# Optimization experiments

Measured on AMD Instinct MI355X. Metric: run time of the kernel, lower is better.

## Reference

```python
import jax, jax.numpy as jnp
import numpy as np

M = 4096        # node_num
NN = 16         # neighbors per node (nn_num)
G = 4           # graph_num
IN_F = 32
OUT_F = 32
LOC_F = 8
LHID = 128
B = 16


def setup_inputs() -> dict:
    key = jax.random.key(0)
    ks = jax.random.split(key, 9)
    return {
        "x": jax.random.normal(ks[0], (B, M, IN_F), jnp.float32),
        "maps": jax.random.normal(ks[1], (M * NN, LOC_F), jnp.float32),
        "L_idx": jax.random.randint(ks[2], (M * NN,), 0, M * M, jnp.int64 if jax.config.jax_enable_x64 else jnp.int32),
        "W1": jax.random.normal(ks[3], (G, LHID, LOC_F), jnp.float32) * 0.1,
        "b1": jax.random.normal(ks[4], (G, LHID), jnp.float32) * 0.1,
        "W2": jax.random.normal(ks[5], (G, LHID), jnp.float32) * 0.1,
        "b2": jax.random.normal(ks[6], (G,), jnp.float32) * 0.1,
        "Wx": jax.random.normal(ks[7], (G, IN_F, OUT_F), jnp.float32) * 0.1,
        "bx": jax.random.normal(ks[8], (OUT_F,), jnp.float32) * 0.1,
    }


def reference(x, maps, L_idx, W1, b1, W2, b2, Wx, bx):
    # x: (B, m, in_f); maps: (m*nn, loc); L_idx: (m*nn,) indices into flat m*m
    g, lhid, loc = W1.shape
    bsz, m, f = x.shape
    nn_num = maps.shape[0] // m

    # per-graph tiny MLP over all node-neighbor pairs, vectorized over graphs
    h = jnp.tanh(jnp.einsum("nl,ghl->gnh", maps, W1) + b1[:, None, :])   # (g, m*nn, lhid)
    ctx = jnp.einsum("gnh,gh->gn", h, W2) + b2[:, None]                   # (g, m*nn)
    # softmax over the nn_num neighbors of each node (F.softmax on (m, nn) -> dim=1)
    attn = jax.nn.softmax(ctx.reshape(g, m, nn_num), axis=-1).reshape(g, m * nn_num)

    # scatter attention into dense per-graph Laplacians: L[L_idx] = attn
    L = jnp.zeros((g, m * m), attn.dtype).at[:, L_idx].set(attn).reshape(g, m, m)

    # XeLayer: out = sum_g (L_g @ x) @ Wx_g + bx
    agg = jnp.einsum("gij,bjf->gbif", L, x)          # (g, B, m, f)
    out = jnp.einsum("gbif,gfo->bio", agg, Wx) + bx   # (B, m, out_f)
    return out
```

## Files before the change

### kernel.cpp

```cpp
#include <hip/hip_runtime.h>

#define M_NODES 4096
#define NN_NUM 16
#define G_NUM 4
#define IN_F 32
#define OUT_F 32
#define LOC_F 8
#define LHID 128
#define B_SZ 16
#define NPAIR 65536
#define ROWCAP 64

typedef __attribute__((ext_vector_type(8))) short short8;
typedef __attribute__((ext_vector_type(4))) float f32x4;

static __device__ __forceinline__ unsigned short f2bf(float f) {
  union { float f; unsigned u; } c; c.f = f;
  const unsigned r = c.u + 0x7FFFu + ((c.u >> 16) & 1u);
  return (unsigned short)(r >> 16);
}
static __device__ __forceinline__ float bfhi2f(unsigned u) {
  union { unsigned u; float f; } c; c.u = u & 0xFFFF0000u; return c.f;
}
static __device__ __forceinline__ float bflo2f(unsigned u) {
  union { unsigned u; float f; } c; c.u = u << 16; return c.f;
}

__global__ void __launch_bounds__(256)
prep_kernel(const float* __restrict__ maps,
            const float* __restrict__ W1,
            const float* __restrict__ b1,
            const float* __restrict__ W2,
            const float* __restrict__ Wx,
            uint4* __restrict__ mapsbf4,
            ushort* __restrict__ w1bf,
            float2* __restrict__ b1w2,
            ushort4* __restrict__ wxf4,
            unsigned* __restrict__ rowcount) {
  const int idx = blockIdx.x * 256 + threadIdx.x;

  {
    const float4 a = *reinterpret_cast<const float4*>(maps + (size_t)idx * 8);
    const float4 b = *reinterpret_cast<const float4*>(maps + (size_t)idx * 8 + 4);
    uint4 r;
    r.x = (unsigned)f2bf(a.x) | ((unsigned)f2bf(a.y) << 16);
    r.y = (unsigned)f2bf(a.z) | ((unsigned)f2bf(a.w) << 16);
    r.z = (unsigned)f2bf(b.x) | ((unsigned)f2bf(b.y) << 16);
    r.w = (unsigned)f2bf(b.z) | ((unsigned)f2bf(b.w) << 16);
    mapsbf4[idx] = r;
  }

  if (idx < G_NUM * LHID * LOC_F) w1bf[idx] = f2bf(W1[idx]);
  if (idx < G_NUM * LHID)
    b1w2[idx] = make_float2(b1[idx], -2.0f * W2[idx]);

  if (idx < 512) {
    const int l = idx & 63, tile = (idx >> 6) & 1, g = idx >> 7;
    const int lo = l & 15, hi = l >> 4;
    ushort4 r0, r1;
    r0.x = f2bf(Wx[g * 1024 + (hi * 8 + 0) * 32 + tile * 16 + lo]);
    r0.y = f2bf(Wx[g * 1024 + (hi * 8 + 1) * 32 + tile * 16 + lo]);
    r0.z = f2bf(Wx[g * 1024 + (hi * 8 + 2) * 32 + tile * 16 + lo]);
    r0.w = f2bf(Wx[g * 1024 + (hi * 8 + 3) * 32 + tile * 16 + lo]);
    r1.x = f2bf(Wx[g * 1024 + (hi * 8 + 4) * 32 + tile * 16 + lo]);
    r1.y = f2bf(Wx[g * 1024 + (hi * 8 + 5) * 32 + tile * 16 + lo]);
    r1.z = f2bf(Wx[g * 1024 + (hi * 8 + 6) * 32 + tile * 16 + lo]);
    r1.w = f2bf(Wx[g * 1024 + (hi * 8 + 7) * 32 + tile * 16 + lo]);
    wxf4[idx * 2] = r0;
    wxf4[idx * 2 + 1] = r1;
  }

  if (idx < M_NODES) rowcount[idx] = 0;
}

__global__ void __launch_bounds__(256)
mlp_kernel(const float4* __restrict__ x4,
           ushort4* __restrict__ xb4,
           const ushort* __restrict__ mapsbf,
           const ushort* __restrict__ w1bf,
           const float2* __restrict__ b1w2,
           const int* __restrict__ L_idx,
           unsigned* __restrict__ rowcount,
           uint2* __restrict__ csr_jn,
           float4* __restrict__ csr_a) {
  const int t = threadIdx.x;
  const int l = t & 63;
  const int g = t >> 6;
  const int node = blockIdx.x;
  const int lo = l & 15;
  const int hi = l >> 4;

  __shared__ float sAttn[G_NUM][16];

  {
    const int idx = blockIdx.x * 256 + t;
    if (idx < 524288) {
      const float4 v = x4[idx];
      ushort4 o;
      o.x = f2bf(v.x); o.y = f2bf(v.y); o.z = f2bf(v.z); o.w = f2bf(v.w);
      xb4[idx] = o;
    }
  }

  short8 aF = {0, 0, 0, 0, 0, 0, 0, 0};
  if (hi == 0)
    aF = *reinterpret_cast<const short8*>(mapsbf + ((size_t)node * 16 + lo) * 8);

  short8 bF[8];
  float2 bw[8];
#pragma unroll
  for (int tile = 0; tile < 8; ++tile) {
    bF[tile] = *reinterpret_cast<const short8*>(
        w1bf + ((size_t)(g * LHID + tile * 16 + lo)) * 8);
    bw[tile] = b1w2[g * LHID + tile * 16 + lo];
  }

  float cr[4] = {0.f, 0.f, 0.f, 0.f};
#pragma unroll
  for (int tile = 0; tile < 8; ++tile) {
    f32x4 c = {bw[tile].x, bw[tile].x, bw[tile].x, bw[tile].x};
    c = __builtin_amdgcn_mfma_f32_16x16x32_bf16(aF, bF[tile], c, 0, 0, 0);
    const float nw2 = bw[tile].y;
#pragma unroll
    for (int r = 0; r < 4; ++r) {
      const float e = __expf(c[r] + c[r]);
      cr[r] = fmaf(nw2, __builtin_amdgcn_rcpf(e + 1.0f), cr[r]);
    }
  }

#pragma unroll
  for (int m = 1; m <= 8; m <<= 1) {
    cr[0] += __shfl_xor(cr[0], m, 64);
    cr[1] += __shfl_xor(cr[1], m, 64);
    cr[2] += __shfl_xor(cr[2], m, 64);
    cr[3] += __shfl_xor(cr[3], m, 64);
  }

  float mx = fmaxf(fmaxf(cr[0], cr[1]), fmaxf(cr[2], cr[3]));
  mx = fmaxf(mx, __shfl_xor(mx, 16, 64));
  mx = fmaxf(mx, __shfl_xor(mx, 32, 64));
  const float e0 = __expf(cr[0] - mx), e1 = __expf(cr[1] - mx);
  const float e2 = __expf(cr[2] - mx), e3 = __expf(cr[3] - mx);
  float s = e0 + e1 + e2 + e3;
  s += __shfl_xor(s, 16, 64);
  s += __shfl_xor(s, 32, 64);
  const float inv = __builtin_amdgcn_rcpf(s);

  if (lo == 0) {
    sAttn[g][hi * 4 + 0] = e0 * inv;
    sAttn[g][hi * 4 + 1] = e1 * inv;
    sAttn[g][hi * 4 + 2] = e2 * inv;
    sAttn[g][hi * 4 + 3] = e3 * inv;
  }
  __syncthreads();

  if (t < 16) {
    const int n = node * 16 + t;
    const unsigned pos = (unsigned)L_idx[n];
    const unsigned i = pos >> 12;
    const unsigned j = pos & (M_NODES - 1);
    const unsigned slot = atomicAdd(&rowcount[i], 1u);
    if (slot < ROWCAP) {
      csr_jn[(size_t)i * ROWCAP + slot] = make_uint2(j, (unsigned)n);
      csr_a[(size_t)i * ROWCAP + slot] =
          make_float4(sAttn[0][t], sAttn[1][t], sAttn[2][t], sAttn[3][t]);
    }
  }
}

__global__ void __launch_bounds__(256)
gather_kernel(const ushort* __restrict__ xbf,
              const uint2* __restrict__ csr_jn,
              const float4* __restrict__ csr_a,
              const unsigned* __restrict__ rowcount,
              const ushort* __restrict__ wxf,
              const float* __restrict__ bx,
              float* __restrict__ out) {
  const int t = threadIdx.x;
  const int l = t & 63;
  const int i = blockIdx.x * 4 + (t >> 6);
  const int lo = l & 15;
  const int hi = l >> 4;

  short8 bF[G_NUM][2];
#pragma unroll
  for (int g = 0; g < G_NUM; ++g)
#pragma unroll
    for (int tile = 0; tile < 2; ++tile)
      bF[g][tile] = *reinterpret_cast<const short8*>(
          wxf + ((size_t)((g * 2 + tile) * 64 + l)) * 8);

  const unsigned cnt = min(rowcount[i], (unsigned)ROWCAP);
  const uint2 e = csr_jn[(size_t)i * ROWCAP + l];
  float4 aq = csr_a[(size_t)i * ROWCAP + l];
  const bool valid = (unsigned)l < cnt;
  unsigned myj = valid ? e.x : 0xFFFFFFFFu;
  const unsigned myn = valid ? e.y : 0u;

  bool alive = valid;
  for (unsigned d = 0; d < cnt; ++d) {
    const unsigned jd = __shfl(myj, (int)d);
    const unsigned nd = __shfl(myn, (int)d);
    if (jd == myj && nd > myn) alive = false;
  }
  if (!alive) { aq.x = 0.f; aq.y = 0.f; aq.z = 0.f; aq.w = 0.f; }
  myj &= (M_NODES - 1u);

  float acc[G_NUM][8];
#pragma unroll
  for (int g = 0; g < G_NUM; ++g)
#pragma unroll
    for (int q = 0; q < 8; ++q) acc[g][q] = 0.f;

  const uint4* xrow = reinterpret_cast<const uint4*>(xbf) + hi;
  const size_t browbase = (size_t)lo * M_NODES * 4;

  for (unsigned s = 0; s < cnt; ++s) {
    const unsigned js = __shfl(myj, (int)s);
    const float w0 = __shfl(aq.x, (int)s);
    const float w1 = __shfl(aq.y, (int)s);
    const float w2 = __shfl(aq.z, (int)s);
    const float w3 = __shfl(aq.w, (int)s);
    const uint4 xv = xrow[browbase + (size_t)js * 4];
    float xf[8];
    xf[0] = bflo2f(xv.x); xf[1] = bfhi2f(xv.x);
    xf[2] = bflo2f(xv.y); xf[3] = bfhi2f(xv.y);
    xf[4] = bflo2f(xv.z); xf[5] = bfhi2f(xv.z);
    xf[6] = bflo2f(xv.w); xf[7] = bfhi2f(xv.w);
#pragma unroll
    for (int q = 0; q < 8; ++q) {
      acc[0][q] = fmaf(w0, xf[q], acc[0][q]);
      acc[1][q] = fmaf(w1, xf[q], acc[1][q]);
      acc[2][q] = fmaf(w2, xf[q], acc[2][q]);
      acc[3][q] = fmaf(w3, xf[q], acc[3][q]);
    }
  }

  f32x4 c0 = {0.f, 0.f, 0.f, 0.f};
  f32x4 c1 = {0.f, 0.f, 0.f, 0.f};
#pragma unroll
  for (int g = 0; g < G_NUM; ++g) {
    short8 aF;
#pragma unroll
    for (int q = 0; q < 8; ++q) aF[q] = (short)f2bf(acc[g][q]);
    c0 = __builtin_amdgcn_mfma_f32_16x16x32_bf16(aF, bF[g][0], c0, 0, 0, 0);
    c1 = __builtin_amdgcn_mfma_f32_16x16x32_bf16(aF, bF[g][1], c1, 0, 0, 0);
  }

  const float bias0 = bx[lo];
  const float bias1 = bx[16 + lo];
#pragma unroll
  for (int r = 0; r < 4; ++r) {
    const int b = hi * 4 + r;
    float* op = out + ((size_t)b * M_NODES + i) * OUT_F;
    op[lo] = c0[r] + bias0;
    op[16 + lo] = c1[r] + bias1;
  }
}

extern "C" void kernel_launch(void* const* d_in, const int* in_sizes, int n_in,
                              void* d_out, int out_size, void* d_ws, size_t ws_size,
                              hipStream_t stream) {
  const float* x    = (const float*)d_in[0];
  const float* maps = (const float*)d_in[1];
  const int*   L_idx = (const int*)d_in[2];
  const float* W1   = (const float*)d_in[3];
  const float* b1   = (const float*)d_in[4];
  const float* W2   = (const float*)d_in[5];
  const float* Wx   = (const float*)d_in[7];
  const float* bx   = (const float*)d_in[8];
  float* out = (float*)d_out;

  char* ws = (char*)d_ws;
  float4*   csr_a    = (float4*)ws;
  uint2*    csr_jn   = (uint2*)(ws + (4u << 20));
  ushort*   xbf      = (ushort*)(ws + (6u << 20));
  unsigned* rowcount = (unsigned*)(ws + (10u << 20));
  ushort*   mapsbf   = (ushort*)(ws + (11u << 20));
  ushort*   w1bf     = (ushort*)(ws + (12u << 20));
  float2*   b1w2     = (float2*)(ws + (12u << 20) + (32u << 10));
  ushort*   wxf      = (ushort*)(ws + (12u << 20) + (64u << 10));

  prep_kernel<<<256, 256, 0, stream>>>(
      maps, W1, b1, W2, Wx,
      (uint4*)mapsbf, w1bf, b1w2, (ushort4*)wxf, rowcount);
  mlp_kernel<<<M_NODES, 256, 0, stream>>>(
      (const float4*)x, (ushort4*)xbf, mapsbf, w1bf, b1w2, L_idx,
      rowcount, csr_jn, csr_a);
  gather_kernel<<<M_NODES / 4, 256, 0, stream>>>(
      xbf, csr_jn, csr_a, rowcount, wxf, bx, out);
}
```

Measured before the change: 44.18 us.

## Process two nodes per MLP block and batch gather loads in groups of eight

```diff
diff --git a/kernel.cpp b/kernel.cpp
--- a/kernel.cpp
+++ b/kernel.cpp
@@ -86,25 +86,26 @@
   const int t = threadIdx.x;
   const int l = t & 63;
   const int g = t >> 6;
-  const int node = blockIdx.x;
+  const int node0 = blockIdx.x * 2;
   const int lo = l & 15;
   const int hi = l >> 4;
 
-  __shared__ float sAttn[G_NUM][16];
+  __shared__ float sAttn[G_NUM][2][16];
 
   {
     const int idx = blockIdx.x * 256 + t;
-    if (idx < 524288) {
-      const float4 v = x4[idx];
-      ushort4 o;
-      o.x = f2bf(v.x); o.y = f2bf(v.y); o.z = f2bf(v.z); o.w = f2bf(v.w);
-      xb4[idx] = o;
-    }
-  }
-
-  short8 aF = {0, 0, 0, 0, 0, 0, 0, 0};
-  if (hi == 0)
-    aF = *reinterpret_cast<const short8*>(mapsbf + ((size_t)node * 16 + lo) * 8);
+    const float4 v = x4[idx];
+    ushort4 o;
+    o.x = f2bf(v.x); o.y = f2bf(v.y); o.z = f2bf(v.z); o.w = f2bf(v.w);
+    xb4[idx] = o;
+  }
+
+  short8 aF0 = {0, 0, 0, 0, 0, 0, 0, 0};
+  short8 aF1 = {0, 0, 0, 0, 0, 0, 0, 0};
+  if (hi == 0) {
+    aF0 = *reinterpret_cast<const short8*>(mapsbf + ((size_t)node0 * 16 + lo) * 8);
+    aF1 = *reinterpret_cast<const short8*>(mapsbf + ((size_t)(node0 + 1) * 16 + lo) * 8);
+  }
 
   short8 bF[8];
   float2 bw[8];
@@ -115,47 +116,67 @@
     bw[tile] = b1w2[g * LHID + tile * 16 + lo];
   }
 
-  float cr[4] = {0.f, 0.f, 0.f, 0.f};
+  float cr0[4] = {0.f, 0.f, 0.f, 0.f};
+  float cr1[4] = {0.f, 0.f, 0.f, 0.f};
 #pragma unroll
   for (int tile = 0; tile < 8; ++tile) {
-    f32x4 c = {bw[tile].x, bw[tile].x, bw[tile].x, bw[tile].x};
-    c = __builtin_amdgcn_mfma_f32_16x16x32_bf16(aF, bF[tile], c, 0, 0, 0);
+    const float b1v = bw[tile].x;
     const float nw2 = bw[tile].y;
+    f32x4 c0 = {b1v, b1v, b1v, b1v};
+    f32x4 c1 = {b1v, b1v, b1v, b1v};
+    c0 = __builtin_amdgcn_mfma_f32_16x16x32_bf16(aF0, bF[tile], c0, 0, 0, 0);
+    c1 = __builtin_amdgcn_mfma_f32_16x16x32_bf16(aF1, bF[tile], c1, 0, 0, 0);
 #pragma unroll
     for (int r = 0; r < 4; ++r) {
-      const float e = __expf(c[r] + c[r]);
-      cr[r] = fmaf(nw2, __builtin_amdgcn_rcpf(e + 1.0f), cr[r]);
+      const float e0 = exp2f(c0[r] * 2.885390082f);
+      const float e1 = exp2f(c1[r] * 2.885390082f);
+      cr0[r] = fmaf(nw2, __builtin_amdgcn_rcpf(e0 + 1.0f), cr0[r]);
+      cr1[r] = fmaf(nw2, __builtin_amdgcn_rcpf(e1 + 1.0f), cr1[r]);
     }
   }
 
 #pragma unroll
   for (int m = 1; m <= 8; m <<= 1) {
-    cr[0] += __shfl_xor(cr[0], m, 64);
-    cr[1] += __shfl_xor(cr[1], m, 64);
-    cr[2] += __shfl_xor(cr[2], m, 64);
-    cr[3] += __shfl_xor(cr[3], m, 64);
-  }
-
-  float mx = fmaxf(fmaxf(cr[0], cr[1]), fmaxf(cr[2], cr[3]));
-  mx = fmaxf(mx, __shfl_xor(mx, 16, 64));
-  mx = fmaxf(mx, __shfl_xor(mx, 32, 64));
-  const float e0 = __expf(cr[0] - mx), e1 = __expf(cr[1] - mx);
-  const float e2 = __expf(cr[2] - mx), e3 = __expf(cr[3] - mx);
-  float s = e0 + e1 + e2 + e3;
-  s += __shfl_xor(s, 16, 64);
-  s += __shfl_xor(s, 32, 64);
-  const float inv = __builtin_amdgcn_rcpf(s);
+#pragma unroll
+    for (int r = 0; r < 4; ++r) {
+      cr0[r] += __shfl_xor(cr0[r], m, 64);
+      cr1[r] += __shfl_xor(cr1[r], m, 64);
+    }
+  }
+
+  float mx0 = fmaxf(fmaxf(cr0[0], cr0[1]), fmaxf(cr0[2], cr0[3]));
+  float mx1 = fmaxf(fmaxf(cr1[0], cr1[1]), fmaxf(cr1[2], cr1[3]));
+  mx0 = fmaxf(mx0, __shfl_xor(mx0, 16, 64));
+  mx1 = fmaxf(mx1, __shfl_xor(mx1, 16, 64));
+  mx0 = fmaxf(mx0, __shfl_xor(mx0, 32, 64));
+  mx1 = fmaxf(mx1, __shfl_xor(mx1, 32, 64));
+  float e00 = __expf(cr0[0] - mx0), e01 = __expf(cr0[1] - mx0);
+  float e02 = __expf(cr0[2] - mx0), e03 = __expf(cr0[3] - mx0);
+  float e10 = __expf(cr1[0] - mx1), e11 = __expf(cr1[1] - mx1);
+  float e12 = __expf(cr1[2] - mx1), e13 = __expf(cr1[3] - mx1);
+  float s0 = e00 + e01 + e02 + e03;
+  float s1 = e10 + e11 + e12 + e13;
+  s0 += __shfl_xor(s0, 16, 64); s1 += __shfl_xor(s1, 16, 64);
+  s0 += __shfl_xor(s0, 32, 64); s1 += __shfl_xor(s1, 32, 64);
+  const float inv0 = __builtin_amdgcn_rcpf(s0);
+  const float inv1 = __builtin_amdgcn_rcpf(s1);
 
   if (lo == 0) {
-    sAttn[g][hi * 4 + 0] = e0 * inv;
-    sAttn[g][hi * 4 + 1] = e1 * inv;
-    sAttn[g][hi * 4 + 2] = e2 * inv;
-    sAttn[g][hi * 4 + 3] = e3 * inv;
+    sAttn[g][0][hi * 4 + 0] = e00 * inv0;
+    sAttn[g][0][hi * 4 + 1] = e01 * inv0;
+    sAttn[g][0][hi * 4 + 2] = e02 * inv0;
+    sAttn[g][0][hi * 4 + 3] = e03 * inv0;
+    sAttn[g][1][hi * 4 + 0] = e10 * inv1;
+    sAttn[g][1][hi * 4 + 1] = e11 * inv1;
+    sAttn[g][1][hi * 4 + 2] = e12 * inv1;
+    sAttn[g][1][hi * 4 + 3] = e13 * inv1;
   }
   __syncthreads();
 
-  if (t < 16) {
-    const int n = node * 16 + t;
+  if (t < 32) {
+    const int ns = t >> 4;
+    const int p = t & 15;
+    const int n = (node0 + ns) * 16 + p;
     const unsigned pos = (unsigned)L_idx[n];
     const unsigned i = pos >> 12;
     const unsigned j = pos & (M_NODES - 1);
@@ -163,7 +184,8 @@
     if (slot < ROWCAP) {
       csr_jn[(size_t)i * ROWCAP + slot] = make_uint2(j, (unsigned)n);
       csr_a[(size_t)i * ROWCAP + slot] =
-          make_float4(sAttn[0][t], sAttn[1][t], sAttn[2][t], sAttn[3][t]);
+          make_float4(sAttn[0][ns][p], sAttn[1][ns][p],
+                      sAttn[2][ns][p], sAttn[3][ns][p]);
     }
   }
 }
@@ -182,14 +204,6 @@
   const int lo = l & 15;
   const int hi = l >> 4;
 
-  short8 bF[G_NUM][2];
-#pragma unroll
-  for (int g = 0; g < G_NUM; ++g)
-#pragma unroll
-    for (int tile = 0; tile < 2; ++tile)
-      bF[g][tile] = *reinterpret_cast<const short8*>(
-          wxf + ((size_t)((g * 2 + tile) * 64 + l)) * 8);
-
   const unsigned cnt = min(rowcount[i], (unsigned)ROWCAP);
   const uint2 e = csr_jn[(size_t)i * ROWCAP + l];
   float4 aq = csr_a[(size_t)i * ROWCAP + l];
@@ -215,26 +229,42 @@
   const uint4* xrow = reinterpret_cast<const uint4*>(xbf) + hi;
   const size_t browbase = (size_t)lo * M_NODES * 4;
 
-  for (unsigned s = 0; s < cnt; ++s) {
-    const unsigned js = __shfl(myj, (int)s);
-    const float w0 = __shfl(aq.x, (int)s);
-    const float w1 = __shfl(aq.y, (int)s);
-    const float w2 = __shfl(aq.z, (int)s);
-    const float w3 = __shfl(aq.w, (int)s);
-    const uint4 xv = xrow[browbase + (size_t)js * 4];
-    float xf[8];
-    xf[0] = bflo2f(xv.x); xf[1] = bfhi2f(xv.x);
-    xf[2] = bflo2f(xv.y); xf[3] = bfhi2f(xv.y);
-    xf[4] = bflo2f(xv.z); xf[5] = bfhi2f(xv.z);
-    xf[6] = bflo2f(xv.w); xf[7] = bfhi2f(xv.w);
-#pragma unroll
-    for (int q = 0; q < 8; ++q) {
-      acc[0][q] = fmaf(w0, xf[q], acc[0][q]);
-      acc[1][q] = fmaf(w1, xf[q], acc[1][q]);
-      acc[2][q] = fmaf(w2, xf[q], acc[2][q]);
-      acc[3][q] = fmaf(w3, xf[q], acc[3][q]);
+  const unsigned cnt8 = (cnt + 7u) & ~7u;
+  for (unsigned base = 0; base < cnt8; base += 8) {
+    unsigned js[8];
+    uint4 v[8];
+#pragma unroll
+    for (int k = 0; k < 8; ++k) js[k] = __shfl(myj, (int)(base + k));
+#pragma unroll
+    for (int k = 0; k < 8; ++k) v[k] = xrow[browbase + (size_t)js[k] * 4];
+#pragma unroll
+    for (int k = 0; k < 8; ++k) {
+      const float w0 = __shfl(aq.x, (int)(base + k));
+      const float w1 = __shfl(aq.y, (int)(base + k));
+      const float w2 = __shfl(aq.z, (int)(base + k));
+      const float w3 = __shfl(aq.w, (int)(base + k));
+      float xf[8];
+      xf[0] = bflo2f(v[k].x); xf[1] = bfhi2f(v[k].x);
+      xf[2] = bflo2f(v[k].y); xf[3] = bfhi2f(v[k].y);
+      xf[4] = bflo2f(v[k].z); xf[5] = bfhi2f(v[k].z);
+      xf[6] = bflo2f(v[k].w); xf[7] = bfhi2f(v[k].w);
+#pragma unroll
+      for (int q = 0; q < 8; ++q) {
+        acc[0][q] = fmaf(w0, xf[q], acc[0][q]);
+        acc[1][q] = fmaf(w1, xf[q], acc[1][q]);
+        acc[2][q] = fmaf(w2, xf[q], acc[2][q]);
+        acc[3][q] = fmaf(w3, xf[q], acc[3][q]);
+      }
     }
   }
+
+  short8 bF[G_NUM][2];
+#pragma unroll
+  for (int g = 0; g < G_NUM; ++g)
+#pragma unroll
+    for (int tile = 0; tile < 2; ++tile)
+      bF[g][tile] = *reinterpret_cast<const short8*>(
+          wxf + ((size_t)((g * 2 + tile) * 64 + l)) * 8);
 
   f32x4 c0 = {0.f, 0.f, 0.f, 0.f};
   f32x4 c1 = {0.f, 0.f, 0.f, 0.f};
@@ -284,7 +314,7 @@
   prep_kernel<<<256, 256, 0, stream>>>(
       maps, W1, b1, W2, Wx,
       (uint4*)mapsbf, w1bf, b1w2, (ushort4*)wxf, rowcount);
-  mlp_kernel<<<M_NODES, 256, 0, stream>>>(
+  mlp_kernel<<<M_NODES / 2, 256, 0, stream>>>(
       (const float4*)x, (ushort4*)xbf, mapsbf, w1bf, b1w2, L_idx,
       rowcount, csr_jn, csr_a);
   gather_kernel<<<M_NODES / 4, 256, 0, stream>>>(
```

Result: slower. 50.21 us (+13.6%).

## Pipeline gather row loads through LDS with async global_load_lds staging

Applied to the files above, without the earlier changes.

```diff
diff --git a/kernel.cpp b/kernel.cpp
--- a/kernel.cpp
+++ b/kernel.cpp
@@ -10,9 +10,12 @@
 #define B_SZ 16
 #define NPAIR 65536
 #define ROWCAP 64
+#define STAGE_D 4
 
 typedef __attribute__((ext_vector_type(8))) short short8;
 typedef __attribute__((ext_vector_type(4))) float f32x4;
+typedef const unsigned __attribute__((address_space(1))) gbl_u32;
+typedef unsigned __attribute__((address_space(3))) lds_u32;
 
 static __device__ __forceinline__ unsigned short f2bf(float f) {
   union { float f; unsigned u; } c; c.f = f;
@@ -118,12 +121,13 @@
   float cr[4] = {0.f, 0.f, 0.f, 0.f};
 #pragma unroll
   for (int tile = 0; tile < 8; ++tile) {
-    f32x4 c = {bw[tile].x, bw[tile].x, bw[tile].x, bw[tile].x};
+    const float b1v = bw[tile].x;
+    const float nw2 = bw[tile].y;
+    f32x4 c = {b1v, b1v, b1v, b1v};
     c = __builtin_amdgcn_mfma_f32_16x16x32_bf16(aF, bF[tile], c, 0, 0, 0);
-    const float nw2 = bw[tile].y;
 #pragma unroll
     for (int r = 0; r < 4; ++r) {
-      const float e = __expf(c[r] + c[r]);
+      const float e = exp2f(c[r] * 2.885390082f);
       cr[r] = fmaf(nw2, __builtin_amdgcn_rcpf(e + 1.0f), cr[r]);
     }
   }
@@ -178,17 +182,12 @@
               float* __restrict__ out) {
   const int t = threadIdx.x;
   const int l = t & 63;
-  const int i = blockIdx.x * 4 + (t >> 6);
+  const int w = t >> 6;
+  const int i = blockIdx.x * 4 + w;
   const int lo = l & 15;
   const int hi = l >> 4;
 
-  short8 bF[G_NUM][2];
-#pragma unroll
-  for (int g = 0; g < G_NUM; ++g)
-#pragma unroll
-    for (int tile = 0; tile < 2; ++tile)
-      bF[g][tile] = *reinterpret_cast<const short8*>(
-          wxf + ((size_t)((g * 2 + tile) * 64 + l)) * 8);
+  __shared__ uint4 sStage[4][STAGE_D][64];
 
   const unsigned cnt = min(rowcount[i], (unsigned)ROWCAP);
   const uint2 e = csr_jn[(size_t)i * ROWCAP + l];
@@ -206,22 +205,51 @@
   if (!alive) { aq.x = 0.f; aq.y = 0.f; aq.z = 0.f; aq.w = 0.f; }
   myj &= (M_NODES - 1u);
 
+  short8 bF[G_NUM][2];
+#pragma unroll
+  for (int g = 0; g < G_NUM; ++g)
+#pragma unroll
+    for (int tile = 0; tile < 2; ++tile)
+      bF[g][tile] = *reinterpret_cast<const short8*>(
+          wxf + ((size_t)((g * 2 + tile) * 64 + l)) * 8);
+  const float bias0 = bx[lo];
+  const float bias1 = bx[16 + lo];
+  asm volatile("s_waitcnt vmcnt(0)" ::: "memory");
+
   float acc[G_NUM][8];
 #pragma unroll
   for (int g = 0; g < G_NUM; ++g)
 #pragma unroll
     for (int q = 0; q < 8; ++q) acc[g][q] = 0.f;
 
-  const uint4* xrow = reinterpret_cast<const uint4*>(xbf) + hi;
-  const size_t browbase = (size_t)lo * M_NODES * 4;
-
-  for (unsigned s = 0; s < cnt; ++s) {
-    const unsigned js = __shfl(myj, (int)s);
-    const float w0 = __shfl(aq.x, (int)s);
-    const float w1 = __shfl(aq.y, (int)s);
-    const float w2 = __shfl(aq.z, (int)s);
-    const float w3 = __shfl(aq.w, (int)s);
-    const uint4 xv = xrow[browbase + (size_t)js * 4];
+  const char* lanebase =
+      (const char*)xbf + ((size_t)lo * M_NODES) * 64 + (size_t)hi * 16;
+  uint4* mySlots = &sStage[w][0][0];
+
+#define ISSUE_ROW(idx)                                                        \
+  do {                                                                        \
+    const unsigned js_ = __shfl(myj, (int)(idx));                             \
+    __builtin_amdgcn_global_load_lds(                                         \
+        (gbl_u32*)(lanebase + (size_t)js_ * 64),                              \
+        (lds_u32*)(mySlots + ((idx) & (STAGE_D - 1)) * 64), 16, 0, 0);        \
+  } while (0)
+
+  const int icnt = (int)cnt;
+  const int pre = icnt < (STAGE_D - 1) ? icnt : (STAGE_D - 1);
+  for (int s = 0; s < pre; ++s) ISSUE_ROW(s);
+
+  for (int s = 0; s < icnt; ++s) {
+    if (s + STAGE_D - 1 < icnt) {
+      ISSUE_ROW(s + STAGE_D - 1);
+      asm volatile("s_waitcnt vmcnt(3)" ::: "memory");
+    } else {
+      asm volatile("s_waitcnt vmcnt(0)" ::: "memory");
+    }
+    const uint4 xv = mySlots[(s & (STAGE_D - 1)) * 64 + l];
+    const float w0 = __shfl(aq.x, s);
+    const float w1 = __shfl(aq.y, s);
+    const float w2 = __shfl(aq.z, s);
+    const float w3 = __shfl(aq.w, s);
     float xf[8];
     xf[0] = bflo2f(xv.x); xf[1] = bfhi2f(xv.x);
     xf[2] = bflo2f(xv.y); xf[3] = bfhi2f(xv.y);
@@ -235,6 +263,7 @@
       acc[3][q] = fmaf(w3, xf[q], acc[3][q]);
     }
   }
+#undef ISSUE_ROW
 
   f32x4 c0 = {0.f, 0.f, 0.f, 0.f};
   f32x4 c1 = {0.f, 0.f, 0.f, 0.f};
@@ -247,8 +276,6 @@
     c1 = __builtin_amdgcn_mfma_f32_16x16x32_bf16(aF, bF[g][1], c1, 0, 0, 0);
   }
 
-  const float bias0 = bx[lo];
-  const float bias1 = bx[16 + lo];
 #pragma unroll
   for (int r = 0; r < 4; ++r) {
     const int b = hi * 4 + r;
```

Measured after the change: 48.27 us. 1.09x slower.

## Batch gather loads four at a time and move x bf16 conversion into prep

Applied to the files above, without the earlier changes.

```diff
diff --git a/kernel.cpp b/kernel.cpp
--- a/kernel.cpp
+++ b/kernel.cpp
@@ -27,11 +27,13 @@
 }
 
 __global__ void __launch_bounds__(256)
-prep_kernel(const float* __restrict__ maps,
+prep_kernel(const float4* __restrict__ x4,
+            const float* __restrict__ maps,
             const float* __restrict__ W1,
             const float* __restrict__ b1,
             const float* __restrict__ W2,
             const float* __restrict__ Wx,
+            ushort4* __restrict__ xb4,
             uint4* __restrict__ mapsbf4,
             ushort* __restrict__ w1bf,
             float2* __restrict__ b1w2,
@@ -39,7 +41,15 @@
             unsigned* __restrict__ rowcount) {
   const int idx = blockIdx.x * 256 + threadIdx.x;
 
-  {
+#pragma unroll
+  for (int k = 0; k < 2; ++k) {
+    const float4 v = x4[idx + k * 262144];
+    ushort4 o;
+    o.x = f2bf(v.x); o.y = f2bf(v.y); o.z = f2bf(v.z); o.w = f2bf(v.w);
+    xb4[idx + k * 262144] = o;
+  }
+
+  if (idx < NPAIR) {
     const float4 a = *reinterpret_cast<const float4*>(maps + (size_t)idx * 8);
     const float4 b = *reinterpret_cast<const float4*>(maps + (size_t)idx * 8 + 4);
     uint4 r;
@@ -74,9 +84,7 @@
 }
 
 __global__ void __launch_bounds__(256)
-mlp_kernel(const float4* __restrict__ x4,
-           ushort4* __restrict__ xb4,
-           const ushort* __restrict__ mapsbf,
+mlp_kernel(const ushort* __restrict__ mapsbf,
            const ushort* __restrict__ w1bf,
            const float2* __restrict__ b1w2,
            const int* __restrict__ L_idx,
@@ -92,16 +100,6 @@
 
   __shared__ float sAttn[G_NUM][16];
 
-  {
-    const int idx = blockIdx.x * 256 + t;
-    if (idx < 524288) {
-      const float4 v = x4[idx];
-      ushort4 o;
-      o.x = f2bf(v.x); o.y = f2bf(v.y); o.z = f2bf(v.z); o.w = f2bf(v.w);
-      xb4[idx] = o;
-    }
-  }
-
   short8 aF = {0, 0, 0, 0, 0, 0, 0, 0};
   if (hi == 0)
     aF = *reinterpret_cast<const short8*>(mapsbf + ((size_t)node * 16 + lo) * 8);
@@ -118,12 +116,13 @@
   float cr[4] = {0.f, 0.f, 0.f, 0.f};
 #pragma unroll
   for (int tile = 0; tile < 8; ++tile) {
-    f32x4 c = {bw[tile].x, bw[tile].x, bw[tile].x, bw[tile].x};
+    const float b1v = bw[tile].x;
+    const float nw2 = bw[tile].y;
+    f32x4 c = {b1v, b1v, b1v, b1v};
     c = __builtin_amdgcn_mfma_f32_16x16x32_bf16(aF, bF[tile], c, 0, 0, 0);
-    const float nw2 = bw[tile].y;
 #pragma unroll
     for (int r = 0; r < 4; ++r) {
-      const float e = __expf(c[r] + c[r]);
+      const float e = exp2f(c[r] * 2.885390082f);
       cr[r] = fmaf(nw2, __builtin_amdgcn_rcpf(e + 1.0f), cr[r]);
     }
   }
@@ -182,14 +181,6 @@
   const int lo = l & 15;
   const int hi = l >> 4;
 
-  short8 bF[G_NUM][2];
-#pragma unroll
-  for (int g = 0; g < G_NUM; ++g)
-#pragma unroll
-    for (int tile = 0; tile < 2; ++tile)
-      bF[g][tile] = *reinterpret_cast<const short8*>(
-          wxf + ((size_t)((g * 2 + tile) * 64 + l)) * 8);
-
   const unsigned cnt = min(rowcount[i], (unsigned)ROWCAP);
   const uint2 e = csr_jn[(size_t)i * ROWCAP + l];
   float4 aq = csr_a[(size_t)i * ROWCAP + l];
@@ -215,26 +206,42 @@
   const uint4* xrow = reinterpret_cast<const uint4*>(xbf) + hi;
   const size_t browbase = (size_t)lo * M_NODES * 4;
 
-  for (unsigned s = 0; s < cnt; ++s) {
-    const unsigned js = __shfl(myj, (int)s);
-    const float w0 = __shfl(aq.x, (int)s);
-    const float w1 = __shfl(aq.y, (int)s);
-    const float w2 = __shfl(aq.z, (int)s);
-    const float w3 = __shfl(aq.w, (int)s);
-    const uint4 xv = xrow[browbase + (size_t)js * 4];
-    float xf[8];
-    xf[0] = bflo2f(xv.x); xf[1] = bfhi2f(xv.x);
-    xf[2] = bflo2f(xv.y); xf[3] = bfhi2f(xv.y);
-    xf[4] = bflo2f(xv.z); xf[5] = bfhi2f(xv.z);
-    xf[6] = bflo2f(xv.w); xf[7] = bfhi2f(xv.w);
-#pragma unroll
-    for (int q = 0; q < 8; ++q) {
-      acc[0][q] = fmaf(w0, xf[q], acc[0][q]);
-      acc[1][q] = fmaf(w1, xf[q], acc[1][q]);
-      acc[2][q] = fmaf(w2, xf[q], acc[2][q]);
-      acc[3][q] = fmaf(w3, xf[q], acc[3][q]);
+  const unsigned cnt4 = (cnt + 3u) & ~3u;
+  for (unsigned base = 0; base < cnt4; base += 4) {
+    unsigned js[4];
+#pragma unroll
+    for (int k = 0; k < 4; ++k) js[k] = __shfl(myj, (int)(base + k));
+    uint4 v[4];
+#pragma unroll
+    for (int k = 0; k < 4; ++k) v[k] = xrow[browbase + (size_t)js[k] * 4];
+#pragma unroll
+    for (int k = 0; k < 4; ++k) {
+      const float w0 = __shfl(aq.x, (int)(base + k));
+      const float w1 = __shfl(aq.y, (int)(base + k));
+      const float w2 = __shfl(aq.z, (int)(base + k));
+      const float w3 = __shfl(aq.w, (int)(base + k));
+      float xf[8];
+      xf[0] = bflo2f(v[k].x); xf[1] = bfhi2f(v[k].x);
+      xf[2] = bflo2f(v[k].y); xf[3] = bfhi2f(v[k].y);
+      xf[4] = bflo2f(v[k].z); xf[5] = bfhi2f(v[k].z);
+      xf[6] = bflo2f(v[k].w); xf[7] = bfhi2f(v[k].w);
+#pragma unroll
+      for (int q = 0; q < 8; ++q) {
+        acc[0][q] = fmaf(w0, xf[q], acc[0][q]);
+        acc[1][q] = fmaf(w1, xf[q], acc[1][q]);
+        acc[2][q] = fmaf(w2, xf[q], acc[2][q]);
+        acc[3][q] = fmaf(w3, xf[q], acc[3][q]);
+      }
     }
   }
+
+  short8 bF[G_NUM][2];
+#pragma unroll
+  for (int g = 0; g < G_NUM; ++g)
+#pragma unroll
+    for (int tile = 0; tile < 2; ++tile)
+      bF[g][tile] = *reinterpret_cast<const short8*>(
+          wxf + ((size_t)((g * 2 + tile) * 64 + l)) * 8);
 
   f32x4 c0 = {0.f, 0.f, 0.f, 0.f};
   f32x4 c1 = {0.f, 0.f, 0.f, 0.f};
@@ -281,12 +288,11 @@
   float2*   b1w2     = (float2*)(ws + (12u << 20) + (32u << 10));
   ushort*   wxf      = (ushort*)(ws + (12u << 20) + (64u << 10));
 
-  prep_kernel<<<256, 256, 0, stream>>>(
-      maps, W1, b1, W2, Wx,
-      (uint4*)mapsbf, w1bf, b1w2, (ushort4*)wxf, rowcount);
+  prep_kernel<<<1024, 256, 0, stream>>>(
+      (const float4*)x, maps, W1, b1, W2, Wx,
+      (ushort4*)xbf, (uint4*)mapsbf, w1bf, b1w2, (ushort4*)wxf, rowcount);
   mlp_kernel<<<M_NODES, 256, 0, stream>>>(
-      (const float4*)x, (ushort4*)xbf, mapsbf, w1bf, b1w2, L_idx,
-      rowcount, csr_jn, csr_a);
+      mapsbf, w1bf, b1w2, L_idx, rowcount, csr_jn, csr_a);
   gather_kernel<<<M_NODES / 4, 256, 0, stream>>>(
       xbf, csr_jn, csr_a, rowcount, wxf, bx, out);
 }
```

After: 44.98 us. No clear change (+1.8%).
